# Kernel tuning notes

Measured on AMD Instinct MI355X. Metric: run time of the kernel, lower is better.

Reference implementation:

```python
import jax, jax.numpy as jnp
import numpy as np

N = 8192
H = 512
TAU = 0.8
LAM = 0.5
EPS = 1e-8


def setup_inputs() -> dict:
    key = jax.random.key(0)
    k1, k2, k3, k4, k5 = jax.random.split(key, 5)
    xavier_std = 1.414 * np.sqrt(2.0 / (H + H))  # xavier_normal_ with gain=1.414
    return {
        "z_mp": jax.random.normal(k1, (N, H), dtype=jnp.float32),
        "z_sc": jax.random.normal(k2, (N, H), dtype=jnp.float32),
        "pos": jax.random.randint(k3, (N, N), 0, 2, dtype=jnp.int32),
        "W1": (jax.random.normal(k4, (H, H), dtype=jnp.float32) * xavier_std),
        "b1": jnp.zeros((H,), dtype=jnp.float32),
        "W2": (jax.random.normal(k5, (H, H), dtype=jnp.float32) * xavier_std),
        "b2": jnp.zeros((H,), dtype=jnp.float32),
    }


def _proj(z, W1, b1, W2, b2):
    # nn.Linear applies x @ W.T + b
    h = jax.nn.elu(z @ W1.T + b1)
    return h @ W2.T + b2


def _sim(z1, z2, tau):
    # exp(cosine_similarity / tau), computed as in the original:
    # dot(z1, z2.T) / (|z1| |z2|.T) / tau
    n1 = jnp.linalg.norm(z1, axis=-1, keepdims=True)  # [N,1]
    n2 = jnp.linalg.norm(z2, axis=-1, keepdims=True)  # [N,1]
    dot = z1 @ z2.T                                   # [N,N]
    return jnp.exp(dot / (n1 * n2.T) / tau)


def reference(z_mp, z_sc, pos, W1, b1, W2, b2):
    pos_f = pos.astype(jnp.float32)
    zp_mp = _proj(z_mp, W1, b1, W2, b2)
    zp_sc = _proj(z_sc, W1, b1, W2, b2)

    m_mp2sc = _sim(zp_mp, zp_sc, TAU)   # [N,N]
    m_sc2mp = m_mp2sc.T                 # [N,N]

    # row-normalize, masked log-mean (mp -> sc)
    s_mp = m_mp2sc / (jnp.sum(m_mp2sc, axis=1, keepdims=True) + EPS)
    lori_mp = -jnp.mean(jnp.log(jnp.sum(s_mp * pos_f, axis=-1)))

    # row-normalize, masked log-mean (sc -> mp)
    s_sc = m_sc2mp / (jnp.sum(m_sc2mp, axis=1, keepdims=True) + EPS)
    lori_sc = -jnp.mean(jnp.log(jnp.sum(s_sc * pos_f, axis=-1)))

    return LAM * lori_mp + (1.0 - LAM) * lori_sc
```

## Files before the change

### kernel.cpp

```cpp
#include <hip/hip_runtime.h>
#include <stdint.h>


#define NN 8192
#define HH 512
#define TAUF 0.8f
#define EPSF 1e-8f

typedef __attribute__((ext_vector_type(8))) short short8;
typedef __attribute__((ext_vector_type(4))) float f32x4;
typedef __attribute__((ext_vector_type(4))) int i32x4;
typedef __attribute__((ext_vector_type(4))) unsigned short u16x4;
typedef unsigned short u16;
typedef unsigned int u32;
typedef uint8_t u8;

typedef __attribute__((address_space(1))) void GV;
typedef __attribute__((address_space(3))) void LV;

__device__ __forceinline__ void g2l16(const void* g, void* l) {
  __builtin_amdgcn_global_load_lds((const GV*)g, (LV*)l, 16, 0, 0);
}

__device__ __forceinline__ u16 f2bf(float x) {
  u32 u = __builtin_bit_cast(u32, x);
  u = (u + 0x7fffu + ((u >> 16) & 1u)) >> 16;
  return (u16)u;
}

__global__ void cast_kernel(const float* __restrict__ in, u16* __restrict__ out, int n) {
  int i = (blockIdx.x * 256 + threadIdx.x) * 8;
  if (i >= n) return;
  f32x4 a = *(const f32x4*)(in + i);
  f32x4 b = *(const f32x4*)(in + i + 4);
  u16 o[8];
  o[0] = f2bf(a.x); o[1] = f2bf(a.y); o[2] = f2bf(a.z); o[3] = f2bf(a.w);
  o[4] = f2bf(b.x); o[5] = f2bf(b.y); o[6] = f2bf(b.z); o[7] = f2bf(b.w);
  i32x4 v;
  v.x = (int)(o[0] | ((u32)o[1] << 16)); v.y = (int)(o[2] | ((u32)o[3] << 16));
  v.z = (int)(o[4] | ((u32)o[5] << 16)); v.w = (int)(o[6] | ((u32)o[7] << 16));
  *(i32x4*)(out + i) = v;
}

template <int EPI>
__global__ __launch_bounds__(256)
void gemm_proj(const u16* __restrict__ A1, const u16* __restrict__ A2,
               const u16* __restrict__ W, const float* __restrict__ bias,
               void* __restrict__ out1, void* __restrict__ out2) {
  __shared__ __align__(16) u16 As[128 * 32];
  __shared__ __align__(16) u16 Bs[128 * 32];
  const int tid = threadIdx.x;
  const int lane = tid & 63, w = tid >> 6;
  const int lo = lane & 15, quad = lane >> 4;
  const int wy = w >> 1, wx = w & 1;
  const u16* A; char* Out; int m0;
  if (blockIdx.y < 64) { A = A1; Out = (char*)out1; m0 = blockIdx.y * 128; }
  else                 { A = A2; Out = (char*)out2; m0 = (blockIdx.y - 64) * 128; }
  const int n0 = blockIdx.x * 128;
  const int srow = w * 16 + (lane >> 2);
  const int skel = (lane & 3) * 8;
  char* AsB = (char*)As; char* BsB = (char*)Bs;
  f32x4 acc[4][4] = {};

  for (int k0 = 0; k0 < HH; k0 += 32) {
    const u16* ga = A + (size_t)(m0 + srow) * HH + k0 + skel;
    const u16* gb = W + (size_t)(n0 + srow) * HH + k0 + skel;
    g2l16(ga, AsB + w * 1024);
    g2l16(ga + (size_t)64 * HH, AsB + w * 1024 + 4096);
    g2l16(gb, BsB + w * 1024);
    g2l16(gb + (size_t)64 * HH, BsB + w * 1024 + 4096);
    asm volatile("s_waitcnt vmcnt(0)" ::: "memory");
    __syncthreads();
    short8 aF[4], bF[4];
#pragma unroll
    for (int mi = 0; mi < 4; ++mi)
      aF[mi] = *(const short8*)(AsB + (wy * 64 + mi * 16 + lo) * 64 + quad * 16);
#pragma unroll
    for (int ni = 0; ni < 4; ++ni)
      bF[ni] = *(const short8*)(BsB + (wx * 64 + ni * 16 + lo) * 64 + quad * 16);
#pragma unroll
    for (int mi = 0; mi < 4; ++mi)
#pragma unroll
      for (int ni = 0; ni < 4; ++ni)
        acc[mi][ni] = __builtin_amdgcn_mfma_f32_16x16x32_bf16(aF[mi], bF[ni], acc[mi][ni], 0, 0, 0);
    __syncthreads();
  }
#pragma unroll
  for (int mi = 0; mi < 4; ++mi) {
    int rl = wy * 64 + mi * 16 + quad * 4;
#pragma unroll
    for (int ni = 0; ni < 4; ++ni) {
      int cl = wx * 64 + ni * 16 + lo;
      float bv = bias[n0 + cl];
#pragma unroll
      for (int r = 0; r < 4; ++r) {
        float v = acc[mi][ni][r] + bv;
        size_t idx = (size_t)(m0 + rl + r) * HH + (n0 + cl);
        if (EPI == 0) {
          if (v < 0.f) v = __expf(v) - 1.f;
          ((u16*)Out)[idx] = f2bf(v);
        } else {
          ((float*)Out)[idx] = v;
        }
      }
    }
  }
}

__global__ void norm_kernel(const float* __restrict__ zp, u16* __restrict__ out, float scale) {
  const int row = blockIdx.x;
  const int t = threadIdx.x;
  const float* src = zp + (size_t)row * HH;
  f32x4 v = *(const f32x4*)(src + t * 4);
  float ss = v.x * v.x + v.y * v.y + v.z * v.z + v.w * v.w;
#pragma unroll
  for (int d = 1; d < 64; d <<= 1) ss += __shfl_xor(ss, d, 64);
  __shared__ float red[2];
  if ((t & 63) == 0) red[t >> 6] = ss;
  __syncthreads();
  float inv = scale * rsqrtf(red[0] + red[1]);
  u16x4 o;
  o[0] = f2bf(v.x * inv); o[1] = f2bf(v.y * inv);
  o[2] = f2bf(v.z * inv); o[3] = f2bf(v.w * inv);
  *(u16x4*)(out + (size_t)row * HH + t * 4) = o;
}

__global__ __launch_bounds__(256)
void sim_kernel(const u16* __restrict__ Az, const u16* __restrict__ Bz,
                const int* __restrict__ pos,
                float* __restrict__ rowsum, float* __restrict__ posrow,
                float* __restrict__ colsum, float* __restrict__ poscol) {
  __shared__ __align__(16) u16 As[128 * 32];
  __shared__ __align__(16) u16 Bs[128 * 32];
  __shared__ __align__(16) u8 PB[128 * 136];
  const int tid = threadIdx.x;
  const int lane = tid & 63, w = tid >> 6;
  const int lo = lane & 15, quad = lane >> 4;
  const int wy = w >> 1, wx = w & 1;
  const int i0 = blockIdx.y * 128, j0 = blockIdx.x * 128;
  const int srow = w * 16 + (lane >> 2);
  const int skel = (lane & 3) * 8;
  char* AsB = (char*)As; char* BsB = (char*)Bs;
  f32x4 acc[4][4] = {};

  for (int k0 = 0; k0 < HH; k0 += 32) {
    const u16* ga = Az + (size_t)(i0 + srow) * HH + k0 + skel;
    const u16* gb = Bz + (size_t)(j0 + srow) * HH + k0 + skel;
    g2l16(ga, AsB + w * 1024);
    g2l16(ga + (size_t)64 * HH, AsB + w * 1024 + 4096);
    g2l16(gb, BsB + w * 1024);
    g2l16(gb + (size_t)64 * HH, BsB + w * 1024 + 4096);
    asm volatile("s_waitcnt vmcnt(0)" ::: "memory");
    __syncthreads();
    short8 aF[4], bF[4];
#pragma unroll
    for (int mi = 0; mi < 4; ++mi)
      aF[mi] = *(const short8*)(AsB + (wy * 64 + mi * 16 + lo) * 64 + quad * 16);
#pragma unroll
    for (int ni = 0; ni < 4; ++ni)
      bF[ni] = *(const short8*)(BsB + (wx * 64 + ni * 16 + lo) * 64 + quad * 16);
#pragma unroll
    for (int mi = 0; mi < 4; ++mi)
#pragma unroll
      for (int ni = 0; ni < 4; ++ni)
        acc[mi][ni] = __builtin_amdgcn_mfma_f32_16x16x32_bf16(aF[mi], bF[ni], acc[mi][ni], 0, 0, 0);
    __syncthreads();
  }

#pragma unroll
  for (int it = 0; it < 16; ++it) {
    int chunk = tid + it * 256;
    int jl = chunk >> 5;
    int c4 = (chunk & 31) * 4;
    i32x4 p = *(const i32x4*)(pos + (size_t)(j0 + jl) * NN + i0 + c4);
    u32 packed = ((u32)p.x & 1u) | (((u32)p.y & 1u) << 8) |
                 (((u32)p.z & 1u) << 16) | (((u32)p.w & 1u) << 24);
    *(u32*)(PB + jl * 136 + c4) = packed;
  }
  __syncthreads();

#pragma unroll
  for (int mi = 0; mi < 4; ++mi)
#pragma unroll
    for (int ni = 0; ni < 4; ++ni)
#pragma unroll
      for (int r = 0; r < 4; ++r)
        acc[mi][ni][r] = __expf(acc[mi][ni][r]);

  const int rowb = wy * 64 + quad * 4;
  const int colb = wx * 64 + lo;

#pragma unroll
  for (int mi = 0; mi < 4; ++mi) {
    int rl = rowb + mi * 16;
    float rs[4] = {0.f, 0.f, 0.f, 0.f}, pr[4] = {0.f, 0.f, 0.f, 0.f};
#pragma unroll
    for (int ni = 0; ni < 4; ++ni) {
      int cl = colb + ni * 16;
      const int* pg = pos + (size_t)(i0 + rl) * NN + (j0 + cl);
#pragma unroll
      for (int r = 0; r < 4; ++r) {
        float e = acc[mi][ni][r];
        rs[r] += e;
        int pv = pg[(size_t)r * NN];
        pr[r] += pv ? e : 0.0f;
      }
    }
#pragma unroll
    for (int d = 1; d < 16; d <<= 1) {
#pragma unroll
      for (int r = 0; r < 4; ++r) {
        rs[r] += __shfl_xor(rs[r], d, 64);
        pr[r] += __shfl_xor(pr[r], d, 64);
      }
    }
    if (lo == 0) {
#pragma unroll
      for (int r = 0; r < 4; ++r) {
        unsafeAtomicAdd(&rowsum[i0 + rl + r], rs[r]);
        unsafeAtomicAdd(&posrow[i0 + rl + r], pr[r]);
      }
    }
  }

#pragma unroll
  for (int ni = 0; ni < 4; ++ni) {
    int cl = colb + ni * 16;
    float cs = 0.f, pc = 0.f;
#pragma unroll
    for (int mi = 0; mi < 4; ++mi) {
      int rl = rowb + mi * 16;
      u32 pb4 = *(const u32*)(PB + cl * 136 + rl);
#pragma unroll
      for (int r = 0; r < 4; ++r) {
        float e = acc[mi][ni][r];
        cs += e;
        pc += ((pb4 >> (8 * r)) & 1u) ? e : 0.0f;
      }
    }
    cs += __shfl_xor(cs, 16, 64); cs += __shfl_xor(cs, 32, 64);
    pc += __shfl_xor(pc, 16, 64); pc += __shfl_xor(pc, 32, 64);
    if (quad == 0) {
      unsafeAtomicAdd(&colsum[j0 + cl], cs);
      unsafeAtomicAdd(&poscol[j0 + cl], pc);
    }
  }
}

__global__ void final_kernel(const float* __restrict__ rowsum, const float* __restrict__ posrow,
                             const float* __restrict__ colsum, const float* __restrict__ poscol,
                             float* __restrict__ out) {
  float s = 0.f;
  for (int i = threadIdx.x; i < NN; i += 256) {
    s += __logf(posrow[i] / (rowsum[i] + EPSF));
    s += __logf(poscol[i] / (colsum[i] + EPSF));
  }
#pragma unroll
  for (int d = 1; d < 64; d <<= 1) s += __shfl_xor(s, d, 64);
  __shared__ float red[4];
  if ((threadIdx.x & 63) == 0) red[threadIdx.x >> 6] = s;
  __syncthreads();
  if (threadIdx.x == 0)
    out[0] = -0.5f * (red[0] + red[1] + red[2] + red[3]) / (float)NN;
}

extern "C" void kernel_launch(void* const* d_in, const int* in_sizes, int n_in,
                              void* d_out, int out_size, void* d_ws, size_t ws_size,
                              hipStream_t stream) {
  const float* z_mp = (const float*)d_in[0];
  const float* z_sc = (const float*)d_in[1];
  const int* pos = (const int*)d_in[2];
  const float* W1 = (const float*)d_in[3];
  const float* b1 = (const float*)d_in[4];
  const float* W2 = (const float*)d_in[5];
  const float* b2 = (const float*)d_in[6];
  float* out = (float*)d_out;

  char* ws = (char*)d_ws;
  u16* zbA = (u16*)(ws);
  u16* zbB = (u16*)(ws + 8388608);
  u16* W1b = (u16*)(ws + 16777216);
  u16* W2b = (u16*)(ws + 17301504);
  u16* hA  = (u16*)(ws + 17825792);
  u16* hB  = (u16*)(ws + 26214400);
  float* zpA = (float*)(ws + 34603008);
  float* zpB = (float*)(ws + 51380224);
  u16* znA = (u16*)(ws + 68157440);
  u16* znB = (u16*)(ws + 76546048);
  float* rowsum = (float*)(ws + 84934656);
  float* posrow = rowsum + NN;
  float* colsum = rowsum + 2 * NN;
  float* poscol = rowsum + 3 * NN;

  cast_kernel<<<2048, 256, 0, stream>>>(z_mp, zbA, NN * HH);
  cast_kernel<<<2048, 256, 0, stream>>>(z_sc, zbB, NN * HH);
  cast_kernel<<<128, 256, 0, stream>>>(W1, W1b, HH * HH);
  cast_kernel<<<128, 256, 0, stream>>>(W2, W2b, HH * HH);

  dim3 gp(4, 128);
  gemm_proj<0><<<gp, 256, 0, stream>>>(zbA, zbB, W1b, b1, hA, hB);
  gemm_proj<1><<<gp, 256, 0, stream>>>(hA, hB, W2b, b2, zpA, zpB);

  norm_kernel<<<NN, 128, 0, stream>>>(zpA, znA, 1.0f / TAUF);
  norm_kernel<<<NN, 128, 0, stream>>>(zpB, znB, 1.0f);

  hipMemsetAsync(rowsum, 0, 4 * NN * sizeof(float), stream);

  dim3 gs(64, 64);
  sim_kernel<<<gs, 256, 0, stream>>>(znA, znB, pos, rowsum, posrow, colsum, poscol);
  final_kernel<<<1, 256, 0, stream>>>(rowsum, posrow, colsum, poscol, out);
}
```

Before: 624.1 us.

## Pre-pack pos mask into bitmap and remap sim tiles per XCD

Adds a pack kernel that compresses the int32 pos matrix into a 1-bit-per-entry bitmap once. The sim kernel then reads small bitmap words for both the row and transposed column masks, instead of reading the int32 pos tile twice (one pass uncoalesced per element). The block index is also remapped so blocks on the same XCD share row tiles for better L2 reuse. The cost is an extra full pass over the 256MB pos array in the pack kernel, and the bitmap layout adds indexing complexity.

```diff
diff --git a/kernel.cpp b/kernel.cpp
--- a/kernel.cpp
+++ b/kernel.cpp
@@ -6,6 +6,7 @@
 #define HH 512
 #define TAUF 0.8f
 #define EPSF 1e-8f
+#define NW (NN / 32)
 
 typedef __attribute__((ext_vector_type(8))) short short8;
 typedef __attribute__((ext_vector_type(4))) float f32x4;
@@ -13,7 +14,6 @@
 typedef __attribute__((ext_vector_type(4))) unsigned short u16x4;
 typedef unsigned short u16;
 typedef unsigned int u32;
-typedef uint8_t u8;
 
 typedef __attribute__((address_space(1))) void GV;
 typedef __attribute__((address_space(3))) void LV;
@@ -26,6 +26,22 @@
   u32 u = __builtin_bit_cast(u32, x);
   u = (u + 0x7fffu + ((u >> 16) & 1u)) >> 16;
   return (u16)u;
+}
+
+__global__ __launch_bounds__(256)
+void pack_kernel(const int* __restrict__ pos, u32* __restrict__ P) {
+  int gid = blockIdx.x * 256 + threadIdx.x;
+  const int* src = pos + (size_t)gid * 32;
+  u32 w = 0;
+#pragma unroll
+  for (int c = 0; c < 8; ++c) {
+    i32x4 p = *(const i32x4*)(src + c * 4);
+    w |= ((u32)p.x & 1u) << (c * 4);
+    w |= ((u32)p.y & 1u) << (c * 4 + 1);
+    w |= ((u32)p.z & 1u) << (c * 4 + 2);
+    w |= ((u32)p.w & 1u) << (c * 4 + 3);
+  }
+  P[gid] = w;
 }
 
 __global__ void cast_kernel(const float* __restrict__ in, u16* __restrict__ out, int n) {
@@ -127,17 +143,24 @@
 
 __global__ __launch_bounds__(256)
 void sim_kernel(const u16* __restrict__ Az, const u16* __restrict__ Bz,
-                const int* __restrict__ pos,
+                const u32* __restrict__ Pbits,
                 float* __restrict__ rowsum, float* __restrict__ posrow,
                 float* __restrict__ colsum, float* __restrict__ poscol) {
   __shared__ __align__(16) u16 As[128 * 32];
   __shared__ __align__(16) u16 Bs[128 * 32];
-  __shared__ __align__(16) u8 PB[128 * 136];
+  __shared__ u32 PBi[128 * 4];
+  __shared__ u32 PBj[128 * 4];
   const int tid = threadIdx.x;
   const int lane = tid & 63, w = tid >> 6;
   const int lo = lane & 15, quad = lane >> 4;
   const int wy = w >> 1, wx = w & 1;
-  const int i0 = blockIdx.y * 128, j0 = blockIdx.x * 128;
+
+  const int bid = blockIdx.x + (int)gridDim.x * blockIdx.y;
+  const int xcd = bid & 7, s = bid >> 3;
+  const int by = xcd * 8 + (s >> 6);
+  const int bx = s & 63;
+  const int i0 = by * 128, j0 = bx * 128;
+
   const int srow = w * 16 + (lane >> 2);
   const int skel = (lane & 3) * 8;
   char* AsB = (char*)As; char* BsB = (char*)Bs;
@@ -167,17 +190,15 @@
     __syncthreads();
   }
 
-#pragma unroll
-  for (int it = 0; it < 16; ++it) {
-    int chunk = tid + it * 256;
-    int jl = chunk >> 5;
-    int c4 = (chunk & 31) * 4;
-    i32x4 p = *(const i32x4*)(pos + (size_t)(j0 + jl) * NN + i0 + c4);
-    u32 packed = ((u32)p.x & 1u) | (((u32)p.y & 1u) << 8) |
-                 (((u32)p.z & 1u) << 16) | (((u32)p.w & 1u) << 24);
-    *(u32*)(PB + jl * 136 + c4) = packed;
-  }
-  __syncthreads();
+  {
+    int il = tid >> 1, w2 = (tid & 1) * 2;
+    u32 a0 = Pbits[(size_t)(i0 + il) * NW + (j0 >> 5) + w2];
+    u32 a1 = Pbits[(size_t)(i0 + il) * NW + (j0 >> 5) + w2 + 1];
+    u32 b0 = Pbits[(size_t)(j0 + il) * NW + (i0 >> 5) + w2];
+    u32 b1 = Pbits[(size_t)(j0 + il) * NW + (i0 >> 5) + w2 + 1];
+    PBi[il * 4 + w2] = a0; PBi[il * 4 + w2 + 1] = a1;
+    PBj[il * 4 + w2] = b0; PBj[il * 4 + w2 + 1] = b1;
+  }
 
 #pragma unroll
   for (int mi = 0; mi < 4; ++mi)
@@ -187,24 +208,24 @@
       for (int r = 0; r < 4; ++r)
         acc[mi][ni][r] = __expf(acc[mi][ni][r]);
 
+  __syncthreads();
+
   const int rowb = wy * 64 + quad * 4;
   const int colb = wx * 64 + lo;
 
 #pragma unroll
   for (int mi = 0; mi < 4; ++mi) {
     int rl = rowb + mi * 16;
-    float rs[4] = {0.f, 0.f, 0.f, 0.f}, pr[4] = {0.f, 0.f, 0.f, 0.f};
-#pragma unroll
-    for (int ni = 0; ni < 4; ++ni) {
-      int cl = colb + ni * 16;
-      const int* pg = pos + (size_t)(i0 + rl) * NN + (j0 + cl);
-#pragma unroll
-      for (int r = 0; r < 4; ++r) {
-        float e = acc[mi][ni][r];
-        rs[r] += e;
-        int pv = pg[(size_t)r * NN];
-        pr[r] += pv ? e : 0.0f;
-      }
+    float rs[4], pr[4];
+#pragma unroll
+    for (int r = 0; r < 4; ++r) {
+      u32 W0 = PBi[(rl + r) * 4 + wx * 2];
+      u32 W1 = PBi[(rl + r) * 4 + wx * 2 + 1];
+      float e0 = acc[mi][0][r], e1 = acc[mi][1][r];
+      float e2 = acc[mi][2][r], e3 = acc[mi][3][r];
+      rs[r] = (e0 + e1) + (e2 + e3);
+      pr[r] = (((W0 >> lo) & 1u) ? e0 : 0.f) + (((W0 >> (16 + lo)) & 1u) ? e1 : 0.f) +
+              (((W1 >> lo) & 1u) ? e2 : 0.f) + (((W1 >> (16 + lo)) & 1u) ? e3 : 0.f);
     }
 #pragma unroll
     for (int d = 1; d < 16; d <<= 1) {
@@ -226,16 +247,18 @@
 #pragma unroll
   for (int ni = 0; ni < 4; ++ni) {
     int cl = colb + ni * 16;
+    u32 W0 = PBj[cl * 4 + wy * 2];
+    u32 W1 = PBj[cl * 4 + wy * 2 + 1];
     float cs = 0.f, pc = 0.f;
 #pragma unroll
     for (int mi = 0; mi < 4; ++mi) {
-      int rl = rowb + mi * 16;
-      u32 pb4 = *(const u32*)(PB + cl * 136 + rl);
+      u32 W = (mi < 2) ? W0 : W1;
+      int sh = (mi & 1) * 16 + quad * 4;
 #pragma unroll
       for (int r = 0; r < 4; ++r) {
         float e = acc[mi][ni][r];
         cs += e;
-        pc += ((pb4 >> (8 * r)) & 1u) ? e : 0.0f;
+        pc += ((W >> (sh + r)) & 1u) ? e : 0.f;
       }
     }
     cs += __shfl_xor(cs, 16, 64); cs += __shfl_xor(cs, 32, 64);
@@ -291,6 +314,9 @@
   float* posrow = rowsum + NN;
   float* colsum = rowsum + 2 * NN;
   float* poscol = rowsum + 3 * NN;
+  u32* Pbits = (u32*)(ws + 85065728);
+
+  pack_kernel<<<NN * NW / 256, 256, 0, stream>>>(pos, Pbits);
 
   cast_kernel<<<2048, 256, 0, stream>>>(z_mp, zbA, NN * HH);
   cast_kernel<<<2048, 256, 0, stream>>>(z_sc, zbB, NN * HH);
@@ -307,6 +333,6 @@
   hipMemsetAsync(rowsum, 0, 4 * NN * sizeof(float), stream);
 
   dim3 gs(64, 64);
-  sim_kernel<<<gs, 256, 0, stream>>>(znA, znB, pos, rowsum, posrow, colsum, poscol);
+  sim_kernel<<<gs, 256, 0, stream>>>(znA, znB, Pbits, rowsum, posrow, colsum, poscol);
   final_kernel<<<1, 256, 0, stream>>>(rowsum, posrow, colsum, poscol, out);
 }
```

Measured after the change: 730.1 us. 17.0% more time.
